# Kernel tuning notes

Measured on AMD Instinct MI355X. Metric: run time of the kernel, lower is better.

Reference implementation:

```python
import jax, jax.numpy as jnp
import numpy as np

G, N, E, F, D = 4096, 64, 256, 64, 128
H1, H2 = 16, 2
EP = 32768
EPS = 1e-15
MAX_LOGSTD = 10.0


def setup_inputs() -> dict:
    key = jax.random.key(0)
    ks = jax.random.split(key, 16)
    def lin(k, i, o):
        return (jax.random.normal(k, (i, o), jnp.float32) / np.sqrt(i)).astype(jnp.float32)
    inp = {}
    inp["x"] = jax.random.normal(ks[0], (G, N, F), jnp.float32)
    inp["edge_index"] = jax.random.randint(ks[1], (G, 2, E), 0, N, dtype=jnp.int32)
    inp["edge_weight"] = jax.random.uniform(ks[2], (G, E), jnp.float32)
    inp["pos_edges"] = jax.random.randint(ks[3], (2, EP), 0, G, dtype=jnp.int32)
    inp["neg_edges"] = jax.random.randint(ks[4], (2, EP), 0, G, dtype=jnp.int32)
    inp["eps"] = jax.random.normal(ks[5], (G, D), jnp.float32)
    inp["W_gcn1"] = lin(ks[6], F, D); inp["b_gcn1"] = jnp.zeros((D,), jnp.float32)
    inp["W_fc1"] = lin(ks[7], D, H1); inp["b_fc1"] = jnp.zeros((H1,), jnp.float32)
    inp["W_fc2"] = lin(ks[8], H1, H2); inp["b_fc2"] = jnp.zeros((H2,), jnp.float32)
    inp["W_c1"] = lin(ks[9], D, 2 * D); inp["b_c1"] = jnp.zeros((2 * D,), jnp.float32)
    inp["W_mu"] = lin(ks[10], 2 * D, D); inp["b_mu"] = jnp.zeros((D,), jnp.float32)
    inp["W_ls"] = lin(ks[11], 2 * D, D); inp["b_ls"] = jnp.zeros((D,), jnp.float32)
    inp["emb"] = jax.random.normal(ks[12], (G, D), jnp.float32)
    inp["W_lin1"] = lin(ks[13], 2 * D, 2 * D); inp["b_lin1"] = jnp.zeros((2 * D,), jnp.float32)
    inp["W_lin2"] = lin(ks[14], 2 * D, 2 * D); inp["b_lin2"] = jnp.zeros((2 * D,), jnp.float32)
    return inp


def gcn_conv(x, src, dst, w, W, b, n):
    # PyG GCNConv: add self-loops (weight 1), sym-normalize, aggregate at target (col).
    xw = x @ W                                      # [n, out]
    deg = jnp.zeros((n,), xw.dtype).at[dst].add(w) + 1.0
    dinv = jax.lax.rsqrt(deg)
    norm = dinv[src] * w * dinv[dst]
    agg = jnp.zeros_like(xw).at[dst].add(xw[src] * norm[:, None])
    agg = agg + xw * (dinv * dinv)[:, None]         # self-loop term
    return agg + b


def sage_graph(x, ei, w, W_gcn1, b_gcn1, W_fc1, b_fc1, W_fc2, b_fc2):
    src, dst = ei[0], ei[1]
    h = gcn_conv(x, src, dst, w, W_gcn1, b_gcn1, N)          # [N, D]
    a1 = jnp.tanh(h @ W_fc1 + b_fc1)                         # [N, H1]
    S = jax.nn.softmax(a1 @ W_fc2 + b_fc2, axis=1)           # [N, 2]
    # get_laplacian(normalization='sym'): L = I - D^{-1/2} A D^{-1/2}, deg from row
    deg = jnp.zeros((N,), x.dtype).at[src].add(w)
    dinv = jnp.where(deg > 0, jax.lax.rsqrt(jnp.maximum(deg, 1e-30)), 0.0)
    lw = -dinv[src] * w * dinv[dst]
    L = jnp.zeros((N, N), x.dtype).at[src, dst].add(lw) + jnp.eye(N, dtype=x.dtype)
    new_adj = S.T @ (L @ S)                                  # [2, 2]
    norm_adj = new_adj / jnp.maximum(jnp.sum(jnp.abs(new_adj), axis=1, keepdims=True), 1e-12)
    diag = jnp.diagonal(norm_adj)
    pos_penalty = jnp.mean((diag - 1.0) ** 2)                # MSE vs ones(2)
    g_emb = jnp.mean(S.T @ h, axis=0)                        # [D]
    return g_emb, pos_penalty


def gcn_conv_unw(x, src, dst, W, b, n):
    return gcn_conv(x, src, dst, jnp.ones(src.shape, x.dtype), W, b, n)


def reference(x, edge_index, edge_weight, pos_edges, neg_edges, eps,
              W_gcn1, b_gcn1, W_fc1, b_fc1, W_fc2, b_fc2,
              W_c1, b_c1, W_mu, b_mu, W_ls, b_ls, emb,
              W_lin1, b_lin1, W_lin2, b_lin2):
    g_embs, pens = jax.vmap(sage_graph,
                            in_axes=(0, 0, 0, None, None, None, None, None, None))(
        x, edge_index, edge_weight, W_gcn1, b_gcn1, W_fc1, b_fc1, W_fc2, b_fc2)
    positive_penalty = jnp.mean(pens)
    # VGAE encode over graph-level graph (dropout in eval mode = identity)
    ps, pd = pos_edges[0], pos_edges[1]
    h = jax.nn.relu(gcn_conv_unw(g_embs, ps, pd, W_c1, b_c1, G))
    mu = gcn_conv_unw(h, ps, pd, W_mu, b_mu, G)
    logstd = jnp.minimum(gcn_conv_unw(h, ps, pd, W_ls, b_ls, G), MAX_LOGSTD)
    z = mu + eps * jnp.exp(logstd)                            # reparametrize
    zc = jnp.concatenate([emb, z], axis=-1)                   # [G, 2D]
    def pred(ei):
        fx = zc[ei[0]] @ W_lin1 + b_lin1
        fy = zc[ei[1]] @ W_lin2 + b_lin2
        return jax.nn.sigmoid(jnp.sum(fx * fy, axis=1))
    pos_pred = pred(pos_edges)
    neg_pred = pred(neg_edges)
    rec_loss = -jnp.mean(jnp.log(pos_pred + EPS)) - jnp.mean(jnp.log(1.0 - neg_pred + EPS))
    kl = -0.5 * jnp.mean(jnp.sum(1.0 + 2.0 * logstd - mu ** 2 - jnp.exp(2.0 * logstd), axis=1))
    pre_loss = rec_loss + kl / G
    return pre_loss, positive_penalty, pos_pred, neg_pred
```

## Files before the change

kernel.cpp:

```cpp
#include <hip/hip_runtime.h>
#include <hip/hip_bf16.h>
#include <math.h>

#define GG   4096
#define NNODE 64
#define EEDGE 256
#define FFEAT 64
#define DDIM 128
#define EP   32768

__global__ void k_prep(const float* __restrict__ Wg, const float* __restrict__ Wf1,
                       const float* __restrict__ bf1, const float* __restrict__ bg,
                       float* __restrict__ Wgf1, float* __restrict__ bcomb,
                       float* __restrict__ bg32) {
    int t = threadIdx.x;
    for (int o = t; o < 1024; o += 256) {
        int f = o >> 4, j = o & 15;
        float s = 0.f;
        for (int d = 0; d < 128; ++d) s += Wg[f * 128 + d] * Wf1[d * 16 + j];
        Wgf1[o] = s;
    }
    if (t < 16) {
        float s = bf1[t];
        for (int d = 0; d < 128; ++d) s += bg[d] * Wf1[d * 16 + t];
        bcomb[t] = s;
    }
    if (t >= 128) bg32[t - 128] = 32.0f * bg[t - 128];
}

__global__ __launch_bounds__(256) void k_pg(
    const float* __restrict__ x, const int* __restrict__ ei, const float* __restrict__ ew,
    const float* __restrict__ Wgf1, const float* __restrict__ bcomb,
    const float* __restrict__ Wf2, const float* __restrict__ bf2,
    float* __restrict__ Qh, float* __restrict__ pens)
{
    __shared__ __align__(16) float sm[8464];
    float* xs    = sm;
    float* Wgf1s = sm + 4352;
    float* a1s   = sm + 5376;
    int*   srcs  = (int*)(sm + 6400);
    int*   dsts  = (int*)(sm + 6656);
    float* lwx   = sm + 6912;
    int*   lsrc  = (int*)(sm + 7168);
    float* lnrm  = sm + 7424;
    int*   icnt  = (int*)(sm + 7680);
    int*   offs  = (int*)(sm + 7744);
    int*   curs  = (int*)(sm + 7808);
    float* degw  = sm + 7872;
    float* dinvs = sm + 7936;
    float* deg2s = sm + 8000;
    float* dinv2s= sm + 8064;
    float* Ss    = sm + 8128;
    float* Ssum  = sm + 8256;
    float* LSs   = sm + 8320;
    float* bcs   = sm + 8448;

    const int g = blockIdx.x;
    const int t = threadIdx.x;
    const float* xg = x + (size_t)g * 4096;

    {
        const int* eg = ei + (size_t)g * 512;
        srcs[t] = eg[t];
        dsts[t] = eg[256 + t];
        lwx[t]  = ew[(size_t)g * 256 + t];
        for (int i = t; i < 1024; i += 256) {
            int n = i >> 4, k = (i & 15) * 4;
            *(float4*)&xs[n * 68 + k] = *(const float4*)&xg[n * 64 + k];
        }
        for (int i = t; i < 1024; i += 256) Wgf1s[i] = Wgf1[i];
        if (t < 16) bcs[t] = bcomb[t];
        if (t < 64) { icnt[t] = 0; degw[t] = 1.0f; deg2s[t] = 0.0f; }
        if (t < 128) LSs[t] = 0.0f;
    }
    __syncthreads();

    {
        int dd = dsts[t], s = srcs[t];
        float w = lwx[t];
        atomicAdd(&icnt[dd], 1);
        atomicAdd(&degw[dd], w);
        atomicAdd(&deg2s[s], w);
    }
    __syncthreads();

    if (t < 64) {
        int v = icnt[t], own = v;
        for (int o = 1; o < 64; o <<= 1) { int u = __shfl_up(v, o); if (t >= o) v += u; }
        int excl = v - own;
        offs[t] = excl; curs[t] = excl;
        dinvs[t] = rsqrtf(degw[t]);
        float dg = deg2s[t];
        dinv2s[t] = dg > 0.0f ? rsqrtf(fmaxf(dg, 1e-30f)) : 0.0f;
    }
    __syncthreads();

    {
        int s = srcs[t], dd = dsts[t];
        float w = lwx[t];
        int pos = atomicAdd(&curs[dd], 1);
        lsrc[pos] = s;
        lnrm[pos] = dinvs[s] * w * dinvs[dd];
        lwx[t] = -dinv2s[s] * w * dinv2s[dd];
    }
    __syncthreads();

    {
        int n = t >> 2, base = (t & 3) * 16;
        float sc = dinvs[n] * dinvs[n];
        const float* xrow = &xs[n * 68 + base];
        float4 A0 = *(const float4*)&xrow[0];
        float4 A1 = *(const float4*)&xrow[4];
        float4 A2 = *(const float4*)&xrow[8];
        float4 A3 = *(const float4*)&xrow[12];
        A0.x *= sc; A0.y *= sc; A0.z *= sc; A0.w *= sc;
        A1.x *= sc; A1.y *= sc; A1.z *= sc; A1.w *= sc;
        A2.x *= sc; A2.y *= sc; A2.z *= sc; A2.w *= sc;
        A3.x *= sc; A3.y *= sc; A3.z *= sc; A3.w *= sc;
        int o = offs[n], c = icnt[n];
        for (int j = 0; j < c; ++j) {
            int s = lsrc[o + j];
            float nm = lnrm[o + j];
            const float* xr = &xs[s * 68 + base];
            float4 X0 = *(const float4*)&xr[0];
            float4 X1 = *(const float4*)&xr[4];
            float4 X2 = *(const float4*)&xr[8];
            float4 X3 = *(const float4*)&xr[12];
            A0.x += X0.x * nm; A0.y += X0.y * nm; A0.z += X0.z * nm; A0.w += X0.w * nm;
            A1.x += X1.x * nm; A1.y += X1.y * nm; A1.z += X1.z * nm; A1.w += X1.w * nm;
            A2.x += X2.x * nm; A2.y += X2.y * nm; A2.z += X2.z * nm; A2.w += X2.w * nm;
            A3.x += X3.x * nm; A3.y += X3.y * nm; A3.z += X3.z * nm; A3.w += X3.w * nm;
        }
        __syncthreads();
        float* xw = &xs[n * 68 + base];
        *(float4*)&xw[0]  = A0;
        *(float4*)&xw[4]  = A1;
        *(float4*)&xw[8]  = A2;
        *(float4*)&xw[12] = A3;
    }
    __syncthreads();

    {
        int n = t >> 2, j0 = (t & 3) * 4;
        float a0 = bcs[j0], a1v = bcs[j0 + 1], a2 = bcs[j0 + 2], a3 = bcs[j0 + 3];
#pragma unroll 4
        for (int k4 = 0; k4 < 16; ++k4) {
            float4 hv = *(const float4*)&xs[n * 68 + k4 * 4];
            float4 w0 = *(const float4*)&Wgf1s[(k4 * 4 + 0) * 16 + j0];
            float4 w1 = *(const float4*)&Wgf1s[(k4 * 4 + 1) * 16 + j0];
            float4 w2 = *(const float4*)&Wgf1s[(k4 * 4 + 2) * 16 + j0];
            float4 w3 = *(const float4*)&Wgf1s[(k4 * 4 + 3) * 16 + j0];
            a0  += hv.x * w0.x + hv.y * w1.x + hv.z * w2.x + hv.w * w3.x;
            a1v += hv.x * w0.y + hv.y * w1.y + hv.z * w2.y + hv.w * w3.y;
            a2  += hv.x * w0.z + hv.y * w1.z + hv.z * w2.z + hv.w * w3.z;
            a3  += hv.x * w0.w + hv.y * w1.w + hv.z * w2.w + hv.w * w3.w;
        }
        a1s[n * 16 + j0]     = tanhf(a0);
        a1s[n * 16 + j0 + 1] = tanhf(a1v);
        a1s[n * 16 + j0 + 2] = tanhf(a2);
        a1s[n * 16 + j0 + 3] = tanhf(a3);
    }
    __syncthreads();

    if (t < 128) {
        int n = t >> 1, kk = t & 1;
        float z = bf2[kk];
#pragma unroll
        for (int j = 0; j < 16; ++j) z += a1s[n * 16 + j] * Wf2[j * 2 + kk];
        Ss[n * 2 + kk] = z;
    }
    __syncthreads();

    if (t < 64) {
        float z0 = Ss[t * 2], z1 = Ss[t * 2 + 1];
        float m = fmaxf(z0, z1);
        float e0 = expf(z0 - m), e1 = expf(z1 - m);
        float inv = 1.0f / (e0 + e1);
        e0 *= inv; e1 *= inv;
        Ss[t * 2] = e0; Ss[t * 2 + 1] = e1;
        Ssum[t] = e0 + e1;
    }
    __syncthreads();

    for (int i = t; i < 512; i += 256) {
        int e = i >> 1, kk = i & 1;
        atomicAdd(&LSs[srcs[e] * 2 + kk], lwx[e] * Ss[dsts[e] * 2 + kk]);
    }
    __syncthreads();

    if (t < 64) {
        float s0 = Ss[t * 2], s1 = Ss[t * 2 + 1];
        float l0 = s0 + LSs[t * 2], l1 = s1 + LSs[t * 2 + 1];
        float p00 = s0 * l0, p01 = s0 * l1, p10 = s1 * l0, p11 = s1 * l1;
        for (int o = 32; o; o >>= 1) {
            p00 += __shfl_down(p00, o); p01 += __shfl_down(p01, o);
            p10 += __shfl_down(p10, o); p11 += __shfl_down(p11, o);
        }
        if (t == 0) {
            float r0 = fmaxf(fabsf(p00) + fabsf(p01), 1e-12f);
            float r1 = fmaxf(fabsf(p10) + fabsf(p11), 1e-12f);
            float d0 = p00 / r0 - 1.0f, d1 = p11 / r1 - 1.0f;
            pens[g] = 0.5f * (d0 * d0 + d1 * d1);
        }
    }
    {
        int k = t & 63, p = t >> 6;
        float qk = 0.f;
#pragma unroll 4
        for (int n = p * 16; n < p * 16 + 16; ++n)
            qk += Ssum[n] * xs[n * 68 + k];
        __syncthreads();
        a1s[p * 64 + k] = qk;
    }
    __syncthreads();
    if (t < 64)
        Qh[(size_t)g * 64 + t] = 0.5f * (a1s[t] + a1s[64 + t] + a1s[128 + t] + a1s[192 + t]);
}

__global__ void k_cnt(const int* __restrict__ pd, int* __restrict__ icnt) {
    int e = blockIdx.x * 256 + threadIdx.x;
    atomicAdd(&icnt[pd[e]], 1);
}

__global__ void k_scan(const int* __restrict__ icnt, int* __restrict__ offs,
                       int* __restrict__ curs, float* __restrict__ dinv) {
    __shared__ int wsum[4];
    int t = threadIdx.x;
    int base = t * 16;
    int l0,l1,l2,l3,l4,l5,l6,l7,l8,l9,l10,l11,l12,l13,l14,l15;
    l0=icnt[base+0]; l1=icnt[base+1]; l2=icnt[base+2]; l3=icnt[base+3];
    l4=icnt[base+4]; l5=icnt[base+5]; l6=icnt[base+6]; l7=icnt[base+7];
    l8=icnt[base+8]; l9=icnt[base+9]; l10=icnt[base+10]; l11=icnt[base+11];
    l12=icnt[base+12]; l13=icnt[base+13]; l14=icnt[base+14]; l15=icnt[base+15];
    int s = l0+l1+l2+l3+l4+l5+l6+l7+l8+l9+l10+l11+l12+l13+l14+l15;
    int lane = t & 63, w = t >> 6;
    int v = s;
    for (int o = 1; o < 64; o <<= 1) { int u = __shfl_up(v, o); if (lane >= o) v += u; }
    if (lane == 63) wsum[w] = v;
    __syncthreads();
    int woff = 0;
    for (int i = 0; i < 4; ++i) if (i < w) woff += wsum[i];
    int run = woff + v - s;
#define SC(L, I) offs[base+(I)] = run; curs[base+(I)] = run; \
    dinv[base+(I)] = rsqrtf((float)(L) + 1.0f); run += L;
    SC(l0,0) SC(l1,1) SC(l2,2) SC(l3,3) SC(l4,4) SC(l5,5) SC(l6,6) SC(l7,7)
    SC(l8,8) SC(l9,9) SC(l10,10) SC(l11,11) SC(l12,12) SC(l13,13) SC(l14,14) SC(l15,15)
#undef SC
}

__global__ void k_place(const int* __restrict__ pe, const float* __restrict__ dinv,
                        int* __restrict__ curs, int* __restrict__ csr_src,
                        float* __restrict__ csr_nrm) {
    int e = blockIdx.x * 256 + threadIdx.x;
    int s = pe[e], d = pe[EP + e];
    int pos = atomicAdd(&curs[d], 1);
    csr_src[pos] = s;
    csr_nrm[pos] = dinv[s] * dinv[d];
}

__global__ void k_gather128(const int* __restrict__ offs, const int* __restrict__ icnt,
                            const int* __restrict__ csr_src, const float* __restrict__ csr_nrm,
                            const float* __restrict__ dinv, const float* __restrict__ in,
                            float* __restrict__ out) {
    int g = blockIdx.x, d = threadIdx.x;
    float dv = dinv[g];
    float acc = in[(size_t)g * 128 + d] * dv * dv;
    int o = offs[g], c = icnt[g];
    for (int j = 0; j < c; ++j)
        acc += in[(size_t)csr_src[o + j] * 128 + d] * csr_nrm[o + j];
    out[(size_t)g * 128 + d] = acc;
}

__global__ void k_gather256(const int* __restrict__ offs, const int* __restrict__ icnt,
                            const int* __restrict__ csr_src, const float* __restrict__ csr_nrm,
                            const float* __restrict__ dinv, const float* __restrict__ in,
                            float* __restrict__ out) {
    int g = blockIdx.x, d = threadIdx.x;
    float dv = dinv[g];
    float acc = in[(size_t)g * 256 + d] * dv * dv;
    int o = offs[g], c = icnt[g];
    for (int j = 0; j < c; ++j)
        acc += in[(size_t)csr_src[o + j] * 256 + d] * csr_nrm[o + j];
    out[(size_t)g * 256 + d] = acc;
}

__global__ __launch_bounds__(256) void k_gemm(
    const float* __restrict__ A,
    const float* __restrict__ B0, const float* __restrict__ bias0, float* __restrict__ C0,
    const float* __restrict__ B1, const float* __restrict__ bias1, float* __restrict__ C1,
    int M, int K, int N, int dorelu)
{
    __shared__ __align__(16) float lds[2 * 4352];
    const float* B = B0; const float* bias = bias0; float* C = C0;
    int by = blockIdx.y;
    if (B1 != nullptr && by >= (int)(gridDim.y >> 1)) {
        B = B1; bias = bias1; C = C1; by -= (gridDim.y >> 1);
    }
    const int mb = blockIdx.x * 64, nbb = by * 64;
    const int t = threadIdx.x;
    const int tm4 = (t >> 4) * 4, tn4 = (t & 15) * 4;
    const int ma = t >> 2, ka = (t & 3) * 8;
    const int kb = t >> 3, nb8 = (t & 7) * 8;

    float4 pa0, pa1, pb0, pb1;
#define LOADT(K0) { \
    const float* Ap = &A[(size_t)(mb + ma) * K + (K0) + ka]; \
    pa0 = *(const float4*)Ap; pa1 = *(const float4*)(Ap + 4); \
    const float* Bp = &B[(size_t)((K0) + kb) * N + nbb + nb8]; \
    pb0 = *(const float4*)Bp; pb1 = *(const float4*)(Bp + 4); }
#define STORET(BUF) { \
    float* At_ = lds + (BUF) * 4352; \
    At_[(ka + 0) * 68 + ma] = pa0.x; At_[(ka + 1) * 68 + ma] = pa0.y; \
    At_[(ka + 2) * 68 + ma] = pa0.z; At_[(ka + 3) * 68 + ma] = pa0.w; \
    At_[(ka + 4) * 68 + ma] = pa1.x; At_[(ka + 5) * 68 + ma] = pa1.y; \
    At_[(ka + 6) * 68 + ma] = pa1.z; At_[(ka + 7) * 68 + ma] = pa1.w; \
    float* Bs_ = lds + (BUF) * 4352 + 2176; \
    *(float4*)&Bs_[kb * 68 + nb8] = pb0; *(float4*)&Bs_[kb * 68 + nb8 + 4] = pb1; }

    float4 ca0 = {0,0,0,0}, ca1 = {0,0,0,0}, ca2 = {0,0,0,0}, ca3 = {0,0,0,0};
    const int nk0 = K >> 5;
    LOADT(0)
    STORET(0)
    __syncthreads();
    for (int it = 0; it < nk0; ++it) {
        if (it + 1 < nk0) LOADT((it + 1) * 32)
        const float* At_ = lds + (it & 1) * 4352;
        const float* Bs_ = At_ + 2176;
#pragma unroll
        for (int k = 0; k < 32; ++k) {
            float4 av = *(const float4*)&At_[k * 68 + tm4];
            float4 bv = *(const float4*)&Bs_[k * 68 + tn4];
            ca0.x += av.x * bv.x; ca0.y += av.x * bv.y; ca0.z += av.x * bv.z; ca0.w += av.x * bv.w;
            ca1.x += av.y * bv.x; ca1.y += av.y * bv.y; ca1.z += av.y * bv.z; ca1.w += av.y * bv.w;
            ca2.x += av.z * bv.x; ca2.y += av.z * bv.y; ca2.z += av.z * bv.z; ca2.w += av.z * bv.w;
            ca3.x += av.w * bv.x; ca3.y += av.w * bv.y; ca3.z += av.w * bv.z; ca3.w += av.w * bv.w;
        }
        if (it + 1 < nk0) {
            STORET((it + 1) & 1)
            __syncthreads();
        }
    }
#undef LOADT
#undef STORET
    float4 bv4 = {0, 0, 0, 0};
    if (bias) bv4 = *(const float4*)&bias[nbb + tn4];
#define CST(I, CV) { \
    float4 v; v.x = CV.x + bv4.x; v.y = CV.y + bv4.y; v.z = CV.z + bv4.z; v.w = CV.w + bv4.w; \
    if (dorelu) { v.x = fmaxf(v.x, 0.f); v.y = fmaxf(v.y, 0.f); v.z = fmaxf(v.z, 0.f); v.w = fmaxf(v.w, 0.f); } \
    *(float4*)&C[(size_t)(mb + tm4 + (I)) * N + nbb + tn4] = v; }
    CST(0, ca0) CST(1, ca1) CST(2, ca2) CST(3, ca3)
#undef CST
}

__global__ void k_fin_z(const float* __restrict__ mu_arr, const float* __restrict__ ls_arr,
                        const float* __restrict__ eps, const float* __restrict__ emb,
                        float* __restrict__ zc, float* __restrict__ klp) {
    __shared__ float smw[2];
    int g = blockIdx.x, d = threadIdx.x;
    int idx = g * 128 + d;
    float mu = mu_arr[idx];
    float ls = fminf(ls_arr[idx], 10.0f);
    float z = mu + eps[idx] * expf(ls);
    zc[(size_t)g * 256 + d] = emb[idx];
    zc[(size_t)g * 256 + 128 + d] = z;
    float term = 1.0f + 2.0f * ls - mu * mu - expf(2.0f * ls);
    for (int o = 32; o; o >>= 1) term += __shfl_down(term, o);
    if ((d & 63) == 0) smw[d >> 6] = term;
    __syncthreads();
    if (d == 0) klp[g] = smw[0] + smw[1];
}

__global__ void k_pred(const float* __restrict__ A, const float* __restrict__ B,
                       const int* __restrict__ pos, const int* __restrict__ neg,
                       float* __restrict__ out, float* __restrict__ predp) {
    __shared__ float smw[16];
    int t = threadIdx.x, sub = t >> 4, l = t & 15;
    int eg = blockIdx.x * 16 + sub;
    int isneg = eg >= EP;
    int e = eg - (isneg ? EP : 0);
    const int* eix = isneg ? neg : pos;
    int s = eix[e], d = eix[EP + e];
    const float4* Ar = (const float4*)(A + (size_t)s * 256);
    const float4* Br = (const float4*)(B + (size_t)d * 256);
    float dot = 0.f;
#pragma unroll
    for (int q = 0; q < 4; ++q) {
        float4 av = Ar[l + 16 * q], bv = Br[l + 16 * q];
        dot += av.x * bv.x + av.y * bv.y + av.z * bv.z + av.w * bv.w;
    }
    for (int o = 8; o; o >>= 1) dot += __shfl_down(dot, o);
    if (l == 0) {
        float p = 1.0f / (1.0f + expf(-dot));
        float term;
        if (isneg) { out[2 + EP + e] = p; term = logf(1.0f - p + 1e-15f); }
        else       { out[2 + e] = p;      term = logf(p + 1e-15f); }
        smw[sub] = term;
    }
    __syncthreads();
    if (t == 0) {
        float s16 = 0.f;
#pragma unroll
        for (int i = 0; i < 16; ++i) s16 += smw[i];
        predp[blockIdx.x] = s16;
    }
}

__global__ void k_final(const float* __restrict__ pens, const float* __restrict__ klp,
                        const float* __restrict__ predp, float* __restrict__ out) {
    __shared__ float sm[16];
    int t = threadIdx.x;
    float s_pen = 0.f, s_kl = 0.f, s_pos = 0.f, s_neg = 0.f;
    for (int i = t; i < 4096; i += 256) { s_pen += pens[i]; s_kl += klp[i]; }
    for (int i = t; i < 2048; i += 256) { s_pos += predp[i]; s_neg += predp[2048 + i]; }
    for (int o = 32; o; o >>= 1) {
        s_pen += __shfl_down(s_pen, o); s_kl += __shfl_down(s_kl, o);
        s_pos += __shfl_down(s_pos, o); s_neg += __shfl_down(s_neg, o);
    }
    int w = t >> 6;
    if ((t & 63) == 0) { sm[w] = s_pen; sm[4 + w] = s_kl; sm[8 + w] = s_pos; sm[12 + w] = s_neg; }
    __syncthreads();
    if (t == 0) {
        float pen = sm[0] + sm[1] + sm[2] + sm[3];
        float kls = sm[4] + sm[5] + sm[6] + sm[7];
        float pos = sm[8] + sm[9] + sm[10] + sm[11];
        float neg = sm[12] + sm[13] + sm[14] + sm[15];
        float rec = -(pos / 32768.0f) - (neg / 32768.0f);
        out[0] = rec - 0.5f * kls / (4096.0f * 4096.0f);
        out[1] = pen * (1.0f / 4096.0f);
    }
}

extern "C" void kernel_launch(void* const* d_in, const int* in_sizes, int n_in,
                              void* d_out, int out_size, void* d_ws, size_t ws_size,
                              hipStream_t stream) {
    const float* x   = (const float*)d_in[0];
    const int*   ei  = (const int*)d_in[1];
    const float* ew  = (const float*)d_in[2];
    const int*   pos = (const int*)d_in[3];
    const int*   neg = (const int*)d_in[4];
    const float* eps = (const float*)d_in[5];
    const float* Wg  = (const float*)d_in[6];
    const float* bg  = (const float*)d_in[7];
    const float* Wf1 = (const float*)d_in[8];
    const float* bf1 = (const float*)d_in[9];
    const float* Wf2 = (const float*)d_in[10];
    const float* bf2 = (const float*)d_in[11];
    const float* Wc1 = (const float*)d_in[12];
    const float* bc1 = (const float*)d_in[13];
    const float* Wmu = (const float*)d_in[14];
    const float* bmu = (const float*)d_in[15];
    const float* Wls = (const float*)d_in[16];
    const float* bls = (const float*)d_in[17];
    const float* emb = (const float*)d_in[18];
    const float* Wl1 = (const float*)d_in[19];
    const float* bl1 = (const float*)d_in[20];
    const float* Wl2 = (const float*)d_in[21];
    const float* bl2 = (const float*)d_in[22];
    float* out = (float*)d_out;
    float* ws  = (float*)d_ws;

    float* g_embs  = ws + 0;
    float* dinv    = ws + 524288;
    int*   icnt_g  = (int*)(ws + 528384);
    int*   off_g   = (int*)(ws + 532480);
    int*   cur_g   = (int*)(ws + 536576);
    int*   csr_src = (int*)(ws + 540672);
    float* csr_nrm = ws + 573440;
    float* Qh      = ws + 606208;
    float* ga      = ws + 868352;
    float* h       = ws + 1392640;
    float* ha      = ws + 2441216;
    float* mu_arr  = ws + 3489792;
    float* ls_arr  = ws + 4014080;
    float* zc      = ws + 4538368;
    float* Abuf    = ws + 5586944;
    float* Bbuf    = ws + 6635520;
    float* pens    = ws + 7684096;
    float* klp     = ws + 7688192;
    float* predp   = ws + 7692288;
    float* Wgf1    = ws + 7708672;
    float* bcomb   = ws + 7709696;
    float* bg32    = ws + 7709712;

    hipMemsetAsync(icnt_g, 0, 4096u * 4, stream);

    k_prep<<<1, 256, 0, stream>>>(Wg, Wf1, bf1, bg, Wgf1, bcomb, bg32);
    k_pg<<<GG, 256, 0, stream>>>(x, ei, ew, Wgf1, bcomb, Wf2, bf2, Qh, pens);
    k_gemm<<<dim3(64, 2), 256, 0, stream>>>(Qh, Wg, bg32, g_embs,
                                            nullptr, nullptr, nullptr, GG, 64, 128, 0);

    k_cnt<<<EP / 256, 256, 0, stream>>>(pos + EP, icnt_g);
    k_scan<<<1, 256, 0, stream>>>(icnt_g, off_g, cur_g, dinv);
    k_place<<<EP / 256, 256, 0, stream>>>(pos, dinv, cur_g, csr_src, csr_nrm);

    k_gather128<<<GG, 128, 0, stream>>>(off_g, icnt_g, csr_src, csr_nrm, dinv, g_embs, ga);
    k_gemm<<<dim3(64, 4), 256, 0, stream>>>(ga, Wc1, bc1, h,
                                            nullptr, nullptr, nullptr, GG, 128, 256, 1);

    k_gather256<<<GG, 256, 0, stream>>>(off_g, icnt_g, csr_src, csr_nrm, dinv, h, ha);
    k_gemm<<<dim3(64, 4), 256, 0, stream>>>(ha, Wmu, bmu, mu_arr,
                                            Wls, bls, ls_arr, GG, 256, 128, 0);
    k_fin_z<<<GG, 128, 0, stream>>>(mu_arr, ls_arr, eps, emb, zc, klp);

    k_gemm<<<dim3(64, 8), 256, 0, stream>>>(zc, Wl1, bl1, Abuf,
                                            Wl2, bl2, Bbuf, GG, 256, 256, 0);

    k_pred<<<(2 * EP) / 16, 256, 0, stream>>>(Abuf, Bbuf, pos, neg, out, predp);
    k_final<<<1, 256, 0, stream>>>(pens, klp, predp, out);
}
```

Before: 320.9 us.

## Fuse fc1/fc2/softmax into per-thread register path in k_pg and drop memset

Restructures the per-graph kernel so each of the four threads owning a node computes partial fc1 products from its register-held aggregated features against a permuted Wgf1 layout, reduces them with warp shuffles, then applies tanh, fc2 and softmax in registers. This removes several shared-memory round trips and __syncthreads phases. Edge data also stays in registers instead of shared memory, the softmax row sum (always 1) is folded out of the Q reduction, shared memory per block shrinks, and the global count memset moves into k_prep. In exchange, each thread of a node now redundantly evaluates 16 tanh and the fc2/softmax step, and register pressure rises.

```diff
diff --git a/kernel.cpp b/kernel.cpp
--- a/kernel.cpp
+++ b/kernel.cpp
@@ -12,10 +12,12 @@
 __global__ void k_prep(const float* __restrict__ Wg, const float* __restrict__ Wf1,
                        const float* __restrict__ bf1, const float* __restrict__ bg,
                        float* __restrict__ Wgf1, float* __restrict__ bcomb,
-                       float* __restrict__ bg32) {
+                       float* __restrict__ bg32, int* __restrict__ icnt_g) {
     int t = threadIdx.x;
     for (int o = t; o < 1024; o += 256) {
-        int f = o >> 4, j = o & 15;
+        int r = o >> 4, j = o & 15;
+        int kk = r >> 2, q = r & 3;
+        int f = q * 16 + kk;
         float s = 0.f;
         for (int d = 0; d < 128; ++d) s += Wg[f * 128 + d] * Wf1[d * 16 + j];
         Wgf1[o] = s;
@@ -26,6 +28,7 @@
         bcomb[t] = s;
     }
     if (t >= 128) bg32[t - 128] = 32.0f * bg[t - 128];
+    for (int i = t; i < 4096; i += 256) icnt_g[i] = 0;
 }
 
 __global__ __launch_bounds__(256) void k_pg(
@@ -34,54 +37,50 @@
     const float* __restrict__ Wf2, const float* __restrict__ bf2,
     float* __restrict__ Qh, float* __restrict__ pens)
 {
-    __shared__ __align__(16) float sm[8464];
+    __shared__ __align__(16) float sm[6656];
     float* xs    = sm;
-    float* Wgf1s = sm + 4352;
-    float* a1s   = sm + 5376;
-    int*   srcs  = (int*)(sm + 6400);
-    int*   dsts  = (int*)(sm + 6656);
-    float* lwx   = sm + 6912;
-    int*   lsrc  = (int*)(sm + 7168);
-    float* lnrm  = sm + 7424;
-    int*   icnt  = (int*)(sm + 7680);
-    int*   offs  = (int*)(sm + 7744);
-    int*   curs  = (int*)(sm + 7808);
-    float* degw  = sm + 7872;
-    float* dinvs = sm + 7936;
-    float* deg2s = sm + 8000;
-    float* dinv2s= sm + 8064;
-    float* Ss    = sm + 8128;
-    float* Ssum  = sm + 8256;
-    float* LSs   = sm + 8320;
-    float* bcs   = sm + 8448;
+    float* Wp    = sm + 4352;
+    int*   lsrc  = (int*)(sm + 5376);
+    float* lnrm  = sm + 5632;
+    int*   icnt  = (int*)(sm + 5888);
+    int*   offs  = (int*)(sm + 5952);
+    int*   curs  = (int*)(sm + 6016);
+    float* degw  = sm + 6080;
+    float* dinvs = sm + 6144;
+    float* deg2s = sm + 6208;
+    float* dinv2s= sm + 6272;
+    float* Ss    = sm + 6336;
+    float* LSs   = sm + 6464;
+    float* bcs   = sm + 6592;
+    float* Wf2s  = sm + 6608;
+    float* bf2s  = sm + 6640;
 
     const int g = blockIdx.x;
     const int t = threadIdx.x;
     const float* xg = x + (size_t)g * 4096;
 
+    int es, ed; float wv;
     {
         const int* eg = ei + (size_t)g * 512;
-        srcs[t] = eg[t];
-        dsts[t] = eg[256 + t];
-        lwx[t]  = ew[(size_t)g * 256 + t];
+        es = eg[t];
+        ed = eg[256 + t];
+        wv = ew[(size_t)g * 256 + t];
         for (int i = t; i < 1024; i += 256) {
             int n = i >> 4, k = (i & 15) * 4;
             *(float4*)&xs[n * 68 + k] = *(const float4*)&xg[n * 64 + k];
         }
-        for (int i = t; i < 1024; i += 256) Wgf1s[i] = Wgf1[i];
+        *(float4*)&Wp[t * 4] = *(const float4*)&Wgf1[t * 4];
         if (t < 16) bcs[t] = bcomb[t];
+        if (t < 32) Wf2s[t] = Wf2[t];
+        if (t < 2)  bf2s[t] = bf2[t];
         if (t < 64) { icnt[t] = 0; degw[t] = 1.0f; deg2s[t] = 0.0f; }
         if (t < 128) LSs[t] = 0.0f;
     }
     __syncthreads();
 
-    {
-        int dd = dsts[t], s = srcs[t];
-        float w = lwx[t];
-        atomicAdd(&icnt[dd], 1);
-        atomicAdd(&degw[dd], w);
-        atomicAdd(&deg2s[s], w);
-    }
+    atomicAdd(&icnt[ed], 1);
+    atomicAdd(&degw[ed], wv);
+    atomicAdd(&deg2s[es], wv);
     __syncthreads();
 
     if (t < 64) {
@@ -95,28 +94,26 @@
     }
     __syncthreads();
 
-    {
-        int s = srcs[t], dd = dsts[t];
-        float w = lwx[t];
-        int pos = atomicAdd(&curs[dd], 1);
-        lsrc[pos] = s;
-        lnrm[pos] = dinvs[s] * w * dinvs[dd];
-        lwx[t] = -dinv2s[s] * w * dinv2s[dd];
-    }
-    __syncthreads();
-
-    {
-        int n = t >> 2, base = (t & 3) * 16;
+    float lw;
+    {
+        int pos = atomicAdd(&curs[ed], 1);
+        lsrc[pos] = es;
+        lnrm[pos] = dinvs[es] * wv * dinvs[ed];
+        lw = -dinv2s[es] * wv * dinv2s[ed];
+    }
+    __syncthreads();
+
+    const int n = t >> 2, q = t & 3, base = q * 16;
+    float Av[16];
+    {
         float sc = dinvs[n] * dinvs[n];
         const float* xrow = &xs[n * 68 + base];
-        float4 A0 = *(const float4*)&xrow[0];
-        float4 A1 = *(const float4*)&xrow[4];
-        float4 A2 = *(const float4*)&xrow[8];
-        float4 A3 = *(const float4*)&xrow[12];
-        A0.x *= sc; A0.y *= sc; A0.z *= sc; A0.w *= sc;
-        A1.x *= sc; A1.y *= sc; A1.z *= sc; A1.w *= sc;
-        A2.x *= sc; A2.y *= sc; A2.z *= sc; A2.w *= sc;
-        A3.x *= sc; A3.y *= sc; A3.z *= sc; A3.w *= sc;
+        *(float4*)&Av[0]  = *(const float4*)&xrow[0];
+        *(float4*)&Av[4]  = *(const float4*)&xrow[4];
+        *(float4*)&Av[8]  = *(const float4*)&xrow[8];
+        *(float4*)&Av[12] = *(const float4*)&xrow[12];
+#pragma unroll
+        for (int kk = 0; kk < 16; ++kk) Av[kk] *= sc;
         int o = offs[n], c = icnt[n];
         for (int j = 0; j < c; ++j) {
             int s = lsrc[o + j];
@@ -126,65 +123,60 @@
             float4 X1 = *(const float4*)&xr[4];
             float4 X2 = *(const float4*)&xr[8];
             float4 X3 = *(const float4*)&xr[12];
-            A0.x += X0.x * nm; A0.y += X0.y * nm; A0.z += X0.z * nm; A0.w += X0.w * nm;
-            A1.x += X1.x * nm; A1.y += X1.y * nm; A1.z += X1.z * nm; A1.w += X1.w * nm;
-            A2.x += X2.x * nm; A2.y += X2.y * nm; A2.z += X2.z * nm; A2.w += X2.w * nm;
-            A3.x += X3.x * nm; A3.y += X3.y * nm; A3.z += X3.z * nm; A3.w += X3.w * nm;
+            Av[0]  += X0.x * nm; Av[1]  += X0.y * nm; Av[2]  += X0.z * nm; Av[3]  += X0.w * nm;
+            Av[4]  += X1.x * nm; Av[5]  += X1.y * nm; Av[6]  += X1.z * nm; Av[7]  += X1.w * nm;
+            Av[8]  += X2.x * nm; Av[9]  += X2.y * nm; Av[10] += X2.z * nm; Av[11] += X2.w * nm;
+            Av[12] += X3.x * nm; Av[13] += X3.y * nm; Av[14] += X3.z * nm; Av[15] += X3.w * nm;
         }
         __syncthreads();
         float* xw = &xs[n * 68 + base];
-        *(float4*)&xw[0]  = A0;
-        *(float4*)&xw[4]  = A1;
-        *(float4*)&xw[8]  = A2;
-        *(float4*)&xw[12] = A3;
-    }
-    __syncthreads();
-
-    {
-        int n = t >> 2, j0 = (t & 3) * 4;
-        float a0 = bcs[j0], a1v = bcs[j0 + 1], a2 = bcs[j0 + 2], a3 = bcs[j0 + 3];
-#pragma unroll 4
-        for (int k4 = 0; k4 < 16; ++k4) {
-            float4 hv = *(const float4*)&xs[n * 68 + k4 * 4];
-            float4 w0 = *(const float4*)&Wgf1s[(k4 * 4 + 0) * 16 + j0];
-            float4 w1 = *(const float4*)&Wgf1s[(k4 * 4 + 1) * 16 + j0];
-            float4 w2 = *(const float4*)&Wgf1s[(k4 * 4 + 2) * 16 + j0];
-            float4 w3 = *(const float4*)&Wgf1s[(k4 * 4 + 3) * 16 + j0];
-            a0  += hv.x * w0.x + hv.y * w1.x + hv.z * w2.x + hv.w * w3.x;
-            a1v += hv.x * w0.y + hv.y * w1.y + hv.z * w2.y + hv.w * w3.y;
-            a2  += hv.x * w0.z + hv.y * w1.z + hv.z * w2.z + hv.w * w3.z;
-            a3  += hv.x * w0.w + hv.y * w1.w + hv.z * w2.w + hv.w * w3.w;
-        }
-        a1s[n * 16 + j0]     = tanhf(a0);
-        a1s[n * 16 + j0 + 1] = tanhf(a1v);
-        a1s[n * 16 + j0 + 2] = tanhf(a2);
-        a1s[n * 16 + j0 + 3] = tanhf(a3);
-    }
-    __syncthreads();
-
-    if (t < 128) {
-        int n = t >> 1, kk = t & 1;
-        float z = bf2[kk];
-#pragma unroll
-        for (int j = 0; j < 16; ++j) z += a1s[n * 16 + j] * Wf2[j * 2 + kk];
-        Ss[n * 2 + kk] = z;
-    }
-    __syncthreads();
-
-    if (t < 64) {
-        float z0 = Ss[t * 2], z1 = Ss[t * 2 + 1];
+        *(float4*)&xw[0]  = *(float4*)&Av[0];
+        *(float4*)&xw[4]  = *(float4*)&Av[4];
+        *(float4*)&xw[8]  = *(float4*)&Av[8];
+        *(float4*)&xw[12] = *(float4*)&Av[12];
+    }
+    __syncthreads();
+
+    {
+        float pj[16];
+#pragma unroll
+        for (int j = 0; j < 16; ++j) pj[j] = 0.f;
+#pragma unroll
+        for (int kk = 0; kk < 16; ++kk) {
+            float a = Av[kk];
+            const float* wr = &Wp[((kk << 2) + q) << 4];
+            float4 w0 = *(const float4*)&wr[0];
+            float4 w1 = *(const float4*)&wr[4];
+            float4 w2 = *(const float4*)&wr[8];
+            float4 w3 = *(const float4*)&wr[12];
+            pj[0]  += a * w0.x; pj[1]  += a * w0.y; pj[2]  += a * w0.z; pj[3]  += a * w0.w;
+            pj[4]  += a * w1.x; pj[5]  += a * w1.y; pj[6]  += a * w1.z; pj[7]  += a * w1.w;
+            pj[8]  += a * w2.x; pj[9]  += a * w2.y; pj[10] += a * w2.z; pj[11] += a * w2.w;
+            pj[12] += a * w3.x; pj[13] += a * w3.y; pj[14] += a * w3.z; pj[15] += a * w3.w;
+        }
+#pragma unroll
+        for (int j = 0; j < 16; ++j) {
+            pj[j] += __shfl_xor(pj[j], 1);
+            pj[j] += __shfl_xor(pj[j], 2);
+        }
+        float z0 = bf2s[0], z1 = bf2s[1];
+#pragma unroll
+        for (int j = 0; j < 16; ++j) {
+            float aj = tanhf(pj[j] + bcs[j]);
+            z0 += aj * Wf2s[2 * j];
+            z1 += aj * Wf2s[2 * j + 1];
+        }
         float m = fmaxf(z0, z1);
         float e0 = expf(z0 - m), e1 = expf(z1 - m);
         float inv = 1.0f / (e0 + e1);
-        e0 *= inv; e1 *= inv;
-        Ss[t * 2] = e0; Ss[t * 2 + 1] = e1;
-        Ssum[t] = e0 + e1;
-    }
-    __syncthreads();
-
-    for (int i = t; i < 512; i += 256) {
-        int e = i >> 1, kk = i & 1;
-        atomicAdd(&LSs[srcs[e] * 2 + kk], lwx[e] * Ss[dsts[e] * 2 + kk]);
+        if (q == 0) { Ss[n * 2] = e0 * inv; Ss[n * 2 + 1] = e1 * inv; }
+    }
+    __syncthreads();
+
+    {
+        float s0 = Ss[ed * 2], s1 = Ss[ed * 2 + 1];
+        atomicAdd(&LSs[es * 2],     lw * s0);
+        atomicAdd(&LSs[es * 2 + 1], lw * s1);
     }
     __syncthreads();
 
@@ -207,14 +199,13 @@
         int k = t & 63, p = t >> 6;
         float qk = 0.f;
 #pragma unroll 4
-        for (int n = p * 16; n < p * 16 + 16; ++n)
-            qk += Ssum[n] * xs[n * 68 + k];
-        __syncthreads();
-        a1s[p * 64 + k] = qk;
+        for (int nn = 0; nn < 16; ++nn)
+            qk += xs[(p * 16 + nn) * 68 + k];
+        Wp[p * 64 + k] = qk;
     }
     __syncthreads();
     if (t < 64)
-        Qh[(size_t)g * 64 + t] = 0.5f * (a1s[t] + a1s[64 + t] + a1s[128 + t] + a1s[192 + t]);
+        Qh[(size_t)g * 64 + t] = 0.5f * (Wp[t] + Wp[64 + t] + Wp[128 + t] + Wp[192 + t]);
 }
 
 __global__ void k_cnt(const int* __restrict__ pd, int* __restrict__ icnt) {
@@ -482,9 +473,7 @@
     float* bcomb   = ws + 7709696;
     float* bg32    = ws + 7709712;
 
-    hipMemsetAsync(icnt_g, 0, 4096u * 4, stream);
-
-    k_prep<<<1, 256, 0, stream>>>(Wg, Wf1, bf1, bg, Wgf1, bcomb, bg32);
+    k_prep<<<1, 256, 0, stream>>>(Wg, Wf1, bf1, bg, Wgf1, bcomb, bg32, icnt_g);
     k_pg<<<GG, 256, 0, stream>>>(x, ei, ew, Wgf1, bcomb, Wf2, bf2, Qh, pens);
     k_gemm<<<dim3(64, 2), 256, 0, stream>>>(Qh, Wg, bg32, g_embs,
                                             nullptr, nullptr, nullptr, GG, 64, 128, 0);
```

Measured after the change: 320.4 us. About the same (-0.2%).
